# Kernel optimization log

Hardware: AMD Instinct MI355X
Metric: run time of the kernel (lower is better)

## Reference

```python
import jax, jax.numpy as jnp
import numpy as np

N_E = 1024
E_DIM = 256
TAU = 0.5
BETA = 0.25
LAMB = 0.1
EPS = 1e-10


def setup_inputs() -> dict:
    key = jax.random.key(0)
    k1, k2, k3 = jax.random.split(key, 3)
    z = jax.random.normal(k1, (16, 1024, E_DIM), dtype=jnp.float32)
    # kaiming-normal-initialized codebook (std = sqrt(2 / fan_in))
    emb = jax.random.normal(k2, (N_E, E_DIM), dtype=jnp.float32) * np.sqrt(2.0 / E_DIM)
    u = jax.random.uniform(k3, (16 * 1024, N_E), dtype=jnp.float32)
    return {"z": z, "emb": emb, "u": u}


def reference(z, emb, u):
    zf = z.reshape(-1, E_DIM)                                  # [N, e_dim]
    # squared euclidean distances to each code: ||z||^2 + ||e||^2 - 2 z.e
    d = (jnp.sum(zf * zf, axis=1, keepdims=True)
         + jnp.sum(emb * emb, axis=1)
         - 2.0 * jnp.matmul(zf, emb.T))                        # [N, n_e]
    # gumbel-softmax (hard, straight-through) on logits = -d
    g = -jnp.log(-jnp.log(u + EPS) + EPS)
    y_soft = jax.nn.softmax((-d + g) / TAU, axis=-1)
    idx = jnp.argmax(y_soft, axis=-1)
    y_hard = jax.nn.one_hot(idx, N_E, dtype=y_soft.dtype)
    probs = y_hard + y_soft - jax.lax.stop_gradient(y_soft)    # [N, n_e]
    z_q = jnp.matmul(probs, emb).reshape(z.shape)
    # orthogonality loss on the codebook gram matrix
    gram = jnp.matmul(emb, emb.T)
    ortho = jnp.mean((gram - jnp.eye(N_E, dtype=emb.dtype)) ** 2) / (N_E ** 2)
    emb_loss = jnp.mean((jax.lax.stop_gradient(z_q) - z) ** 2)
    commit = BETA * jnp.mean((z_q - jax.lax.stop_gradient(z)) ** 2)
    loss = emb_loss + BETA * commit + LAMB * ortho
    z_q_st = z + jax.lax.stop_gradient(z_q - z)
    e_mean = jnp.mean(probs, axis=0)
    perplexity = jnp.exp(-jnp.sum(e_mean * jnp.log(e_mean + EPS)))
    return loss, z_q_st, perplexity
```

## Files before the change

### kernel.cpp

```cpp
#include <hip/hip_runtime.h>
#include <math.h>
#include <stdint.h>


#define NROWS 16384
#define NE    1024
#define ED    256
#define EPSF  1e-10f
#define INV2048 4.8828125e-4f
#define BK 64
#define BM 128
#define BN 64
#define SCW 68

typedef _Float16 half_t;
typedef __attribute__((ext_vector_type(4))) _Float16 half4;
typedef __attribute__((ext_vector_type(8))) _Float16 half8;
typedef __attribute__((ext_vector_type(16))) float floatx16;
typedef unsigned long long u64;

__device__ __forceinline__ void gl_lds16(const void* g, void* l) {
    __builtin_amdgcn_global_load_lds(
        (const __attribute__((address_space(1))) uint32_t*)g,
        (__attribute__((address_space(3))) uint32_t*)l, 16, 0, 0);
}

__device__ __forceinline__ u64 packMax(float v, int code) {
    unsigned int b   = __float_as_uint(v);
    unsigned int key = (b & 0x80000000u) ? ~b : (b | 0x80000000u);
    return ((u64)key << 32) | (unsigned int)(NE - 1 - code);
}

__global__ __launch_bounds__(256) void vq_prep(
        const float* __restrict__ z, const float* __restrict__ emb,
        half_t* __restrict__ zh, half_t* __restrict__ zl,
        half_t* __restrict__ eh, half_t* __restrict__ el,
        float* __restrict__ enorm, float* __restrict__ znorm,
        u64* __restrict__ best, int* __restrict__ cnt,
        double* __restrict__ mse_acc, int* __restrict__ done_cnt)
{
    const int gid = blockIdx.x * 256 + threadIdx.x;
    const int ZQ4 = NROWS * ED / 4;
    if (gid < ZQ4) {
        const float4 v = ((const float4*)z)[gid];
        const float x[4] = {v.x, v.y, v.z, v.w};
        half4 h, l;
#pragma unroll
        for (int i = 0; i < 4; ++i) {
            const half_t hi = (half_t)x[i];
            h[i] = hi; l[i] = (half_t)((x[i] - (float)hi) * 2048.0f);
        }
        *(half4*)&zh[(size_t)gid * 4] = h;
        *(half4*)&zl[(size_t)gid * 4] = l;
        float s = v.x*v.x + v.y*v.y + v.z*v.z + v.w*v.w;
#pragma unroll
        for (int o = 32; o; o >>= 1) s += __shfl_down(s, o);
        if ((threadIdx.x & 63) == 0) znorm[gid >> 6] = s;
    } else {
        const int eg = gid - ZQ4;
        const float4 v = ((const float4*)emb)[eg];
        const float x[4] = {v.x, v.y, v.z, v.w};
        half4 h, l;
#pragma unroll
        for (int i = 0; i < 4; ++i) {
            const half_t hi = (half_t)x[i];
            h[i] = hi; l[i] = (half_t)((x[i] - (float)hi) * 2048.0f);
        }
        *(half4*)&eh[(size_t)eg * 4] = h;
        *(half4*)&el[(size_t)eg * 4] = l;
        float s = v.x*v.x + v.y*v.y + v.z*v.z + v.w*v.w;
#pragma unroll
        for (int o = 32; o; o >>= 1) s += __shfl_down(s, o);
        if ((threadIdx.x & 63) == 0) enorm[eg >> 6] = s;
        if (eg < NROWS) best[eg] = 0ull;
        if (eg < NE)    cnt[eg]  = 0;
        if (eg == 0)  { *mse_acc = 0.0; *done_cnt = 0; }
    }
}

__global__ __launch_bounds__(256, 2) void vq_gemm(
        const half_t* __restrict__ zh, const half_t* __restrict__ zl,
        const half_t* __restrict__ eh, const half_t* __restrict__ el,
        const float* __restrict__ u, const float* __restrict__ enorm,
        u64* __restrict__ best)
{
    __shared__ __align__(16) char smem[69632];
    half_t* Ah = (half_t*)smem;
    half_t* Al = (half_t*)(smem + 16384);
    half_t* Bh = (half_t*)(smem + 32768);
    half_t* Bl = (half_t*)(smem + 40960);
    float*  Uf = (float*)smem;
    float (*Sc)[SCW] = (float(*)[SCW])(smem + 32768);
    u64* parr = (u64*)(smem + 67584);

    const int t    = threadIdx.x;
    const int w    = t >> 6;
    const int lane = t & 63;
    const int lrow = lane & 31;
    const int hw   = lane >> 5;

    const int bid = blockIdx.x;
    const int xcd = bid & 7, c = bid >> 3;
    const int m0 = (xcd * 16 + (c >> 4)) * BM;
    const int n0 = (c & 15) * BN;
    const int wm = (w >> 1) * 64, wn = (w & 1) * 32;

    size_t gaoff[4], gboff[2];
#pragma unroll
    for (int it = 0; it < 4; ++it) {
        const int s = it * 256 + t;
        const int row = s >> 3;
        const int cc = (s & 7) ^ (row & 7);
        gaoff[it] = (size_t)(m0 + row) * ED + cc * 8;
    }
#pragma unroll
    for (int it = 0; it < 2; ++it) {
        const int s = it * 256 + t;
        const int row = s >> 3;
        const int cc = (s & 7) ^ (row & 7);
        gboff[it] = (size_t)(n0 + row) * ED + cc * 8;
    }

    auto STAGE = [&](int kc) {
#pragma unroll
        for (int it = 0; it < 4; ++it) {
            const int ldsoff = (it * 256 + w * 64) * 8;
            gl_lds16(zh + gaoff[it] + kc, Ah + ldsoff);
            gl_lds16(zl + gaoff[it] + kc, Al + ldsoff);
        }
#pragma unroll
        for (int it = 0; it < 2; ++it) {
            const int ldsoff = (it * 256 + w * 64) * 8;
            gl_lds16(eh + gboff[it] + kc, Bh + ldsoff);
            gl_lds16(el + gboff[it] + kc, Bl + ldsoff);
        }
    };

    STAGE(0);
    const int   col0 = n0 + wn + lrow;
    const float en0  = enorm[col0];

    floatx16 accH[2] = {};
    floatx16 accX[2] = {};

    for (int kc = 0; kc < ED; kc += BK) {
        __syncthreads();
#pragma unroll
        for (int ks = 0; ks < BK / 16; ++ks) {
            const int cch = ks * 2 + hw;
            const int br = wn + lrow;
            const int sb = br * 8 + (cch ^ (br & 7));
            const half8 bh = *(const half8*)&Bh[sb * 8];
            const half8 bl = *(const half8*)&Bl[sb * 8];
            half8 ah[2], al[2];
#pragma unroll
            for (int i = 0; i < 2; ++i) {
                const int ar = wm + i * 32 + lrow;
                const int sa = ar * 8 + (cch ^ (ar & 7));
                ah[i] = *(const half8*)&Ah[sa * 8];
                al[i] = *(const half8*)&Al[sa * 8];
            }
#pragma unroll
            for (int i = 0; i < 2; ++i) {
                accH[i] = __builtin_amdgcn_mfma_f32_32x32x16_f16(ah[i], bh, accH[i], 0, 0, 0);
                accX[i] = __builtin_amdgcn_mfma_f32_32x32x16_f16(ah[i], bl, accX[i], 0, 0, 0);
                accX[i] = __builtin_amdgcn_mfma_f32_32x32x16_f16(al[i], bh, accX[i], 0, 0, 0);
            }
        }
        __syncthreads();
        if (kc + BK < ED) STAGE(kc + BK);
    }

#pragma unroll
    for (int it = 0; it < 8; ++it) {
        const int s = it * 256 + t;
        const int row = s >> 4, cg = s & 15;
        const int ldsoff = (it * 256 + w * 64) * 4;
        gl_lds16(u + (size_t)(m0 + row) * NE + n0 + cg * 4, Uf + ldsoff);
    }
    __syncthreads();

#pragma unroll
    for (int i = 0; i < 2; ++i) {
#pragma unroll
        for (int r = 0; r < 16; ++r) {
            const int lr = wm + i * 32 + (r & 3) + ((r >> 2) << 3) + (hw << 2);
            const float d  = accH[i][r] + accX[i][r] * INV2048;
            const float uv = Uf[lr * 64 + wn + lrow];
            const float g  = -__logf(-__logf(uv + EPSF) + EPSF);
            Sc[lr][wn + lrow] = 2.f * d - en0 + g;
        }
    }
    __syncthreads();

    {
        const int row = t >> 1;
        const int ch  = (t & 1) << 5;
        float bv = -1e38f; int bc = 0;
#pragma unroll
        for (int q = 0; q < 8; ++q) {
            const float4 v = *(const float4*)&Sc[row][ch + (q << 2)];
            const int cc = n0 + ch + (q << 2);
            if (v.x > bv) { bv = v.x; bc = cc; }
            if (v.y > bv) { bv = v.y; bc = cc + 1; }
            if (v.z > bv) { bv = v.z; bc = cc + 2; }
            if (v.w > bv) { bv = v.w; bc = cc + 3; }
        }
        parr[t] = packMax(bv, bc);
    }
    __syncthreads();
    if (t < 128) {
        const u64 a = parr[t << 1], b = parr[(t << 1) + 1];
        atomicMax(&best[m0 + t], a > b ? a : b);
    }
}

__global__ __launch_bounds__(256) void vq_outfin(
        const float* __restrict__ emb, const float* __restrict__ u,
        const u64* __restrict__ best, const float* __restrict__ znorm,
        int* __restrict__ cnt, double* __restrict__ mse_acc,
        int* __restrict__ done_cnt, float* __restrict__ out)
{
    __shared__ int    ridx[64];
    __shared__ double redd[4];
    __shared__ int    flag;
    const int t  = threadIdx.x;
    const int m0 = blockIdx.x * 64;

    if (t < 64) {
        const u64 p = best[m0 + t];
        const unsigned int key = (unsigned int)(p >> 32);
        const int code = NE - 1 - (int)(p & 0xFFFFFFFFu);
        ridx[t] = code;
        atomicAdd(&cnt[code], 1);
        const unsigned int b = (key & 0x80000000u) ? (key ^ 0x80000000u) : ~key;
        const float s  = __uint_as_float(b);
        const float uv = u[(size_t)(m0 + t) * NE + code];
        const float g  = -__logf(-__logf(uv + EPSF) + EPSF);
        float lm = znorm[m0 + t] - s + g;
#pragma unroll
        for (int o = 32; o; o >>= 1) lm += __shfl_down(lm, o);
        if (t == 0) atomicAdd(mse_acc, (double)lm);
    }
    __syncthreads();

    const int wv = t >> 6, l = t & 63;
#pragma unroll
    for (int rr = 0; rr < 16; ++rr) {
        const int row = (rr << 2) + wv;
        const int j   = ridx[row];
        const size_t ob = 1 + (size_t)(m0 + row) * ED;
        const size_t eb = (size_t)j * ED;
#pragma unroll
        for (int q = 0; q < 4; ++q) {
            const int cc = (q << 6) + l;
            out[ob + cc] = emb[eb + cc];
        }
    }

    if (t == 0) {
        __threadfence();
        flag = (atomicAdd(done_cnt, 1) == NROWS / 64 - 1) ? 1 : 0;
    }
    __syncthreads();
    if (flag) {
        double s = 0.0;
#pragma unroll
        for (int q = 0; q < 4; ++q) {
            const int   cc = atomicAdd(&cnt[(q << 8) + t], 0);
            const float em = (float)cc / (float)NROWS;
            s += (double)(em * logf(em + EPSF));
        }
#pragma unroll
        for (int o = 32; o; o >>= 1) s += __shfl_down(s, o);
        if ((t & 63) == 0) redd[t >> 6] = s;
        __syncthreads();
        if (t == 0) {
            const double tot = redd[0] + redd[1] + redd[2] + redd[3];
            const double mse = atomicAdd(mse_acc, 0.0) / (double)((size_t)NROWS * ED);
            out[0] = (float)(mse * 1.0625);
            out[1 + (size_t)NROWS * ED] = (float)exp(-tot);
        }
    }
}

extern "C" void kernel_launch(void* const* d_in, const int* in_sizes, int n_in,
                              void* d_out, int out_size, void* d_ws, size_t ws_size,
                              hipStream_t stream) {
    const float* z   = (const float*)d_in[0];
    const float* emb = (const float*)d_in[1];
    const float* u   = (const float*)d_in[2];
    float* out = (float*)d_out;

    double* mse_acc  = (double*)d_ws;
    int*    done_cnt = (int*)((char*)d_ws + 64);
    int*    cnt      = (int*)((char*)d_ws + 1024);
    float*  enorm    = (float*)((char*)d_ws + 5120);
    u64*    best     = (u64*)((char*)d_ws + 9216);
    float*  znorm    = (float*)((char*)d_ws + 140288);
    const size_t small_end = 205824;

    const size_t zsplit = (size_t)NROWS * ED * 2;
    const size_t esplit = (size_t)NE * ED * 2;
    const bool bigws = ws_size >= small_end + 2 * zsplit + 2 * esplit;

    half_t *zh, *zl, *eh, *el;
    if (bigws) {
        char* big = (char*)d_ws + small_end;
        zh = (half_t*)big;
        zl = (half_t*)(big + zsplit);
        eh = (half_t*)(big + 2 * zsplit);
        el = (half_t*)(big + 2 * zsplit + esplit);
    } else {
        zh = (half_t*)((char*)d_out + 8);
        zl = (half_t*)((char*)d_out + 8 + zsplit);
        eh = (half_t*)((char*)d_ws + small_end);
        el = (half_t*)((char*)d_ws + small_end + esplit);
    }

    vq_prep<<<(NROWS * ED / 4 + NE * ED / 4) / 256, 256, 0, stream>>>(
        z, emb, zh, zl, eh, el, enorm, znorm, best, cnt, mse_acc, done_cnt);
    vq_gemm<<<(NROWS / BM) * (NE / BN), 256, 0, stream>>>(
        zh, zl, eh, el, u, enorm, best);
    vq_outfin<<<NROWS / 64, 256, 0, stream>>>(
        emb, u, best, znorm, cnt, mse_acc, done_cnt, out);
}
```

Before: 172.2 us.

## Double-buffer GEMM K-loop, prefetch gumbel noise into registers, shrink outfin blocks

```diff
diff --git a/kernel.cpp b/kernel.cpp
--- a/kernel.cpp
+++ b/kernel.cpp
@@ -8,7 +8,6 @@
 #define ED    256
 #define EPSF  1e-10f
 #define INV2048 4.8828125e-4f
-#define BK 64
 #define BM 128
 #define BN 64
 #define SCW 68
@@ -84,14 +83,10 @@
         const float* __restrict__ u, const float* __restrict__ enorm,
         u64* __restrict__ best)
 {
-    __shared__ __align__(16) char smem[69632];
-    half_t* Ah = (half_t*)smem;
-    half_t* Al = (half_t*)(smem + 16384);
-    half_t* Bh = (half_t*)(smem + 32768);
-    half_t* Bl = (half_t*)(smem + 40960);
-    float*  Uf = (float*)smem;
-    float (*Sc)[SCW] = (float(*)[SCW])(smem + 32768);
-    u64* parr = (u64*)(smem + 67584);
+    __shared__ __align__(16) char smem[49152];
+    half_t* SM = (half_t*)smem;
+    float (*Sc)[SCW] = (float(*)[SCW])smem;
+    u64* parr = (u64*)(smem + 34816);
 
     const int t    = threadIdx.x;
     const int w    = t >> 6;
@@ -105,89 +100,96 @@
     const int n0 = (c & 15) * BN;
     const int wm = (w >> 1) * 64, wn = (w & 1) * 32;
 
-    size_t gaoff[4], gboff[2];
-#pragma unroll
-    for (int it = 0; it < 4; ++it) {
-        const int s = it * 256 + t;
-        const int row = s >> 3;
-        const int cc = (s & 7) ^ (row & 7);
-        gaoff[it] = (size_t)(m0 + row) * ED + cc * 8;
-    }
+    size_t gaoff[2]; size_t gboff;
 #pragma unroll
     for (int it = 0; it < 2; ++it) {
         const int s = it * 256 + t;
-        const int row = s >> 3;
-        const int cc = (s & 7) ^ (row & 7);
-        gboff[it] = (size_t)(n0 + row) * ED + cc * 8;
-    }
-
-    auto STAGE = [&](int kc) {
-#pragma unroll
-        for (int it = 0; it < 4; ++it) {
-            const int ldsoff = (it * 256 + w * 64) * 8;
-            gl_lds16(zh + gaoff[it] + kc, Ah + ldsoff);
-            gl_lds16(zl + gaoff[it] + kc, Al + ldsoff);
-        }
+        const int row = s >> 2;
+        const int cc = (s & 3) ^ ((row >> 1) & 3);
+        gaoff[it] = (size_t)(m0 + row) * ED + cc * 8;
+    }
+    {
+        const int row = t >> 2;
+        const int cc = (t & 3) ^ ((row >> 1) & 3);
+        gboff = (size_t)(n0 + row) * ED + cc * 8;
+    }
+
+    auto STAGE = [&](int kt, int b) {
+        half_t* base = SM + b * 12288;
+        const int kh = kt * 32;
 #pragma unroll
         for (int it = 0; it < 2; ++it) {
-            const int ldsoff = (it * 256 + w * 64) * 8;
-            gl_lds16(eh + gboff[it] + kc, Bh + ldsoff);
-            gl_lds16(el + gboff[it] + kc, Bl + ldsoff);
-        }
+            const int ldso = (it * 256 + w * 64) * 8;
+            gl_lds16(zh + gaoff[it] + kh, base + ldso);
+            gl_lds16(zl + gaoff[it] + kh, base + 4096 + ldso);
+        }
+        gl_lds16(eh + gboff + kh, base + 8192  + w * 64 * 8);
+        gl_lds16(el + gboff + kh, base + 10240 + w * 64 * 8);
     };
 
-    STAGE(0);
+    floatx16 accH[2] = {};
+    floatx16 accX[2] = {};
     const int   col0 = n0 + wn + lrow;
     const float en0  = enorm[col0];
-
-    floatx16 accH[2] = {};
-    floatx16 accX[2] = {};
-
-    for (int kc = 0; kc < ED; kc += BK) {
+    float ur[2][16];
+
+    STAGE(0, 0);
+    __syncthreads();
+
+#pragma unroll
+    for (int kt = 0; kt < 8; ++kt) {
+        const int cb = kt & 1;
+        if (kt + 1 < 8) STAGE(kt + 1, cb ^ 1);
+        if (kt == 0) {
+            const float* ub = u + (size_t)(m0 + wm + (hw << 2)) * NE + col0;
+#pragma unroll
+            for (int i = 0; i < 2; ++i)
+#pragma unroll
+                for (int r = 0; r < 16; ++r)
+                    ur[i][r] = ub[(size_t)(i * 32 + (r & 3) + ((r >> 2) << 3)) * NE];
+        }
+        {
+            half_t* base = SM + cb * 12288;
+#pragma unroll
+            for (int ks = 0; ks < 2; ++ks) {
+                const int cch = ks * 2 + hw;
+                const int br = wn + lrow;
+                const int sb = br * 4 + (cch ^ ((br >> 1) & 3));
+                const half8 bh = *(const half8*)&base[8192  + sb * 8];
+                const half8 bl = *(const half8*)&base[10240 + sb * 8];
+                half8 ah[2], al[2];
+#pragma unroll
+                for (int i = 0; i < 2; ++i) {
+                    const int ar = wm + i * 32 + lrow;
+                    const int sa = ar * 4 + (cch ^ ((ar >> 1) & 3));
+                    ah[i] = *(const half8*)&base[sa * 8];
+                    al[i] = *(const half8*)&base[4096 + sa * 8];
+                }
+#pragma unroll
+                for (int i = 0; i < 2; ++i) {
+                    accH[i] = __builtin_amdgcn_mfma_f32_32x32x16_f16(ah[i], bh, accH[i], 0, 0, 0);
+                    accX[i] = __builtin_amdgcn_mfma_f32_32x32x16_f16(ah[i], bl, accX[i], 0, 0, 0);
+                    accX[i] = __builtin_amdgcn_mfma_f32_32x32x16_f16(al[i], bh, accX[i], 0, 0, 0);
+                }
+            }
+        }
+        if (kt == 0) {
+#pragma unroll
+            for (int i = 0; i < 2; ++i)
+#pragma unroll
+                for (int r = 0; r < 16; ++r)
+                    asm volatile("" :: "v"(ur[i][r]));
+        }
         __syncthreads();
-#pragma unroll
-        for (int ks = 0; ks < BK / 16; ++ks) {
-            const int cch = ks * 2 + hw;
-            const int br = wn + lrow;
-            const int sb = br * 8 + (cch ^ (br & 7));
-            const half8 bh = *(const half8*)&Bh[sb * 8];
-            const half8 bl = *(const half8*)&Bl[sb * 8];
-            half8 ah[2], al[2];
-#pragma unroll
-            for (int i = 0; i < 2; ++i) {
-                const int ar = wm + i * 32 + lrow;
-                const int sa = ar * 8 + (cch ^ (ar & 7));
-                ah[i] = *(const half8*)&Ah[sa * 8];
-                al[i] = *(const half8*)&Al[sa * 8];
-            }
-#pragma unroll
-            for (int i = 0; i < 2; ++i) {
-                accH[i] = __builtin_amdgcn_mfma_f32_32x32x16_f16(ah[i], bh, accH[i], 0, 0, 0);
-                accX[i] = __builtin_amdgcn_mfma_f32_32x32x16_f16(ah[i], bl, accX[i], 0, 0, 0);
-                accX[i] = __builtin_amdgcn_mfma_f32_32x32x16_f16(al[i], bh, accX[i], 0, 0, 0);
-            }
-        }
-        __syncthreads();
-        if (kc + BK < ED) STAGE(kc + BK);
-    }
-
-#pragma unroll
-    for (int it = 0; it < 8; ++it) {
-        const int s = it * 256 + t;
-        const int row = s >> 4, cg = s & 15;
-        const int ldsoff = (it * 256 + w * 64) * 4;
-        gl_lds16(u + (size_t)(m0 + row) * NE + n0 + cg * 4, Uf + ldsoff);
-    }
-    __syncthreads();
+    }
 
 #pragma unroll
     for (int i = 0; i < 2; ++i) {
 #pragma unroll
         for (int r = 0; r < 16; ++r) {
             const int lr = wm + i * 32 + (r & 3) + ((r >> 2) << 3) + (hw << 2);
-            const float d  = accH[i][r] + accX[i][r] * INV2048;
-            const float uv = Uf[lr * 64 + wn + lrow];
-            const float g  = -__logf(-__logf(uv + EPSF) + EPSF);
+            const float d = accH[i][r] + accX[i][r] * INV2048;
+            const float g = -__logf(-__logf(ur[i][r] + EPSF) + EPSF);
             Sc[lr][wn + lrow] = 2.f * d - en0 + g;
         }
     }
@@ -221,13 +223,13 @@
         int* __restrict__ cnt, double* __restrict__ mse_acc,
         int* __restrict__ done_cnt, float* __restrict__ out)
 {
-    __shared__ int    ridx[64];
+    __shared__ int    ridx[8];
     __shared__ double redd[4];
     __shared__ int    flag;
     const int t  = threadIdx.x;
-    const int m0 = blockIdx.x * 64;
-
-    if (t < 64) {
+    const int m0 = blockIdx.x * 8;
+
+    if (t < 8) {
         const u64 p = best[m0 + t];
         const unsigned int key = (unsigned int)(p >> 32);
         const int code = NE - 1 - (int)(p & 0xFFFFFFFFu);
@@ -238,29 +240,22 @@
         const float uv = u[(size_t)(m0 + t) * NE + code];
         const float g  = -__logf(-__logf(uv + EPSF) + EPSF);
         float lm = znorm[m0 + t] - s + g;
-#pragma unroll
-        for (int o = 32; o; o >>= 1) lm += __shfl_down(lm, o);
+        lm += __shfl_down(lm, 4);
+        lm += __shfl_down(lm, 2);
+        lm += __shfl_down(lm, 1);
         if (t == 0) atomicAdd(mse_acc, (double)lm);
     }
     __syncthreads();
 
-    const int wv = t >> 6, l = t & 63;
-#pragma unroll
-    for (int rr = 0; rr < 16; ++rr) {
-        const int row = (rr << 2) + wv;
-        const int j   = ridx[row];
-        const size_t ob = 1 + (size_t)(m0 + row) * ED;
-        const size_t eb = (size_t)j * ED;
-#pragma unroll
-        for (int q = 0; q < 4; ++q) {
-            const int cc = (q << 6) + l;
-            out[ob + cc] = emb[eb + cc];
-        }
+#pragma unroll
+    for (int rr = 0; rr < 8; ++rr) {
+        const int j = ridx[rr];
+        out[1 + (size_t)(m0 + rr) * ED + t] = emb[(size_t)j * ED + t];
     }
 
     if (t == 0) {
         __threadfence();
-        flag = (atomicAdd(done_cnt, 1) == NROWS / 64 - 1) ? 1 : 0;
+        flag = (atomicAdd(done_cnt, 1) == NROWS / 8 - 1) ? 1 : 0;
     }
     __syncthreads();
     if (flag) {
@@ -322,6 +317,6 @@
         z, emb, zh, zl, eh, el, enorm, znorm, best, cnt, mse_acc, done_cnt);
     vq_gemm<<<(NROWS / BM) * (NE / BN), 256, 0, stream>>>(
         zh, zl, eh, el, u, enorm, best);
-    vq_outfin<<<NROWS / 64, 256, 0, stream>>>(
+    vq_outfin<<<NROWS / 8, 256, 0, stream>>>(
         emb, u, best, znorm, cnt, mse_acc, done_cnt, out);
 }
```

Result: slower. 257.5 us (+49.5%).
